# Optimization experiments

Measured on AMD Instinct MI355X. Metric: run time of the kernel, lower is better.

Reference implementation:

```python
import jax, jax.numpy as jnp
import numpy as np

N = 50000      # nodes
E = 800000     # edges (avg degree 16)
D_IN, D_H, D_OUT = 128, 256, 128


def setup_inputs() -> dict:
    key = jax.random.key(0)
    ks = jax.random.split(key, 8)
    x = jax.random.normal(ks[0], (N, D_IN), dtype=jnp.float32)
    edge_index = jax.random.randint(ks[1], (2, E), 0, N, dtype=jnp.int64)
    s1 = 1.0 / np.sqrt(D_IN).astype(np.float32)
    s2 = 1.0 / np.sqrt(D_H).astype(np.float32)
    return {
        "x": x,
        "edge_index": edge_index,
        "W1l": jax.random.normal(ks[2], (D_H, D_IN), jnp.float32) * s1,
        "b1l": jnp.zeros((D_H,), jnp.float32),
        "W1r": jax.random.normal(ks[3], (D_H, D_IN), jnp.float32) * s1,
        "W2l": jax.random.normal(ks[4], (D_OUT, D_H), jnp.float32) * s2,
        "b2l": jnp.zeros((D_OUT,), jnp.float32),
        "W2r": jax.random.normal(ks[5], (D_OUT, D_H), jnp.float32) * s2,
    }


def sage_conv(x, src, dst, Wl, bl, Wr):
    # mean-aggregate source features into destination nodes
    agg = jax.ops.segment_sum(x[src], dst, num_segments=N)           # [N, d_in]
    deg = jax.ops.segment_sum(jnp.ones((src.shape[0],), x.dtype), dst, num_segments=N)
    mean = agg / jnp.maximum(deg, 1.0)[:, None]
    # lin_l(mean_agg) + lin_r(x_root); lin_r has no bias (PyG SAGEConv default)
    return mean @ Wl.T + bl + x @ Wr.T


def reference(x, edge_index, W1l, b1l, W1r, W2l, b2l, W2r):
    src, dst = edge_index[0], edge_index[1]
    h = sage_conv(x, src, dst, W1l, b1l, W1r)
    h = jax.nn.relu(h)  # dropout inactive in eval mode
    return sage_conv(h, src, dst, W2l, b2l, W2r)
```

## Files before the change

### kernel.cpp

```cpp
#include <hip/hip_runtime.h>


typedef __attribute__((ext_vector_type(8))) short bf16x8;
typedef __attribute__((ext_vector_type(4))) float floatx4;

__device__ inline unsigned short f2b(float f) {
  unsigned int x = __float_as_uint(f);
  unsigned int r = (x + 0x7fffu + ((x >> 16) & 1u)) >> 16;
  return (unsigned short)r;
}
__device__ inline float blo(unsigned int u) { return __uint_as_float(u << 16); }
__device__ inline float bhi(unsigned int u) { return __uint_as_float(u & 0xffff0000u); }

__global__ void prep_kernel(const float* __restrict__ x,
                            const float* __restrict__ W1l, const float* __restrict__ W1r,
                            const float* __restrict__ W2l, const float* __restrict__ W2r,
                            unsigned short* __restrict__ Wc1, unsigned short* __restrict__ Wc2,
                            unsigned short* __restrict__ A1,
                            int* __restrict__ cnt, int* __restrict__ off, int N, int E) {
  int i = blockIdx.x * blockDim.x + threadIdx.x;
  if (i < 65536) {
    int j = i >> 8, k = i & 255;
    float v1 = (k < 128) ? W1l[j * 128 + k] : W1r[j * 128 + (k - 128)];
    Wc1[i] = f2b(v1);
    float v2 = (j < 128) ? W2l[j * 256 + k] : W2r[(j - 128) * 256 + k];
    Wc2[i] = f2b(v2);
  }
  if (i < N) cnt[i] = 0;
  if (i == 0) off[N] = E;
  if (i < N * 32) {
    int n = i >> 5, c = (i & 31) * 4;
    float4 v = *(const float4*)(x + (size_t)n * 128 + c);
    uint2 p;
    p.x = (unsigned int)f2b(v.x) | ((unsigned int)f2b(v.y) << 16);
    p.y = (unsigned int)f2b(v.z) | ((unsigned int)f2b(v.w) << 16);
    *(uint2*)(A1 + (size_t)n * 256 + 128 + c) = p;
  }
}

__global__ void hist_kernel(const int* __restrict__ dst, int* __restrict__ cnt,
                            int* __restrict__ rank, int E) {
  int i = blockIdx.x * blockDim.x + threadIdx.x;
  int e = i * 4;
  if (e + 3 < E) {
    int4 d = *(const int4*)(dst + e);
    int4 r;
    r.x = atomicAdd(&cnt[d.x], 1);
    r.y = atomicAdd(&cnt[d.y], 1);
    r.z = atomicAdd(&cnt[d.z], 1);
    r.w = atomicAdd(&cnt[d.w], 1);
    *(int4*)(rank + e) = r;
  } else {
    for (; e < E; e++) rank[e] = atomicAdd(&cnt[dst[e]], 1);
  }
}

__global__ __launch_bounds__(1024) void scan_blocks_kernel(const int* __restrict__ cnt,
                                                           int* __restrict__ off,
                                                           int* __restrict__ bsum, int N) {
  __shared__ int wsum[16];
  __shared__ int wincl[16];
  const int tid = threadIdx.x;
  const int lane = tid & 63;
  const int wv = tid >> 6;
  const int i = blockIdx.x * 1024 + tid;
  const int v = (i < N) ? cnt[i] : 0;
  int s = v;
#pragma unroll
  for (int o = 1; o < 64; o <<= 1) {
    int t = __shfl_up(s, o, 64);
    if (lane >= o) s += t;
  }
  if (lane == 63) wsum[wv] = s;
  __syncthreads();
  if (tid < 16) {
    int ws = wsum[tid];
#pragma unroll
    for (int o = 1; o < 16; o <<= 1) {
      int t = __shfl_up(ws, o, 16);
      if ((tid & 15) >= o) ws += t;
    }
    wincl[tid] = ws;
  }
  __syncthreads();
  const int wo = wv ? wincl[wv - 1] : 0;
  if (i < N) off[i] = wo + s - v;
  if (tid == 1023) bsum[blockIdx.x] = wo + s;
}

__global__ __launch_bounds__(1024) void scan_add_kernel(int* __restrict__ off,
                                                        const int* __restrict__ bsum, int N, int SB) {
  __shared__ int bofs[64];
  const int tid = threadIdx.x;
  if (tid < 64) {
    int v = (tid < SB) ? bsum[tid] : 0;
    int s = v;
#pragma unroll
    for (int o = 1; o < 64; o <<= 1) {
      int t = __shfl_up(s, o, 64);
      if (tid >= o) s += t;
    }
    bofs[tid] = s - v;
  }
  __syncthreads();
  int i = blockIdx.x * 1024 + tid;
  if (i < N) off[i] = off[i] + bofs[blockIdx.x];
}

__global__ void fill_kernel(const int* __restrict__ src, const int* __restrict__ dst,
                            const int* __restrict__ rank, const int* __restrict__ off,
                            int* __restrict__ csr, int E) {
  int i = blockIdx.x * blockDim.x + threadIdx.x;
  int e = i * 4;
  if (e + 3 < E) {
    int4 d = *(const int4*)(dst + e);
    int4 r = *(const int4*)(rank + e);
    int4 s = *(const int4*)(src + e);
    csr[off[d.x] + r.x] = s.x;
    csr[off[d.y] + r.y] = s.y;
    csr[off[d.z] + r.z] = s.z;
    csr[off[d.w] + r.w] = s.w;
  } else {
    for (; e < E; e++) csr[off[dst[e]] + rank[e]] = src[e];
  }
}

__global__ void gather1_kernel(const unsigned short* __restrict__ feat,
                               const int* __restrict__ csr, const int* __restrict__ off,
                               unsigned short* __restrict__ ob, int N) {
  int wid = (blockIdx.x * blockDim.x + threadIdx.x) >> 6;
  if (wid >= N) return;
  const int lane = threadIdx.x & 63;
  const int s0 = off[wid], s1 = off[wid + 1];
  float a0 = 0.f, a1 = 0.f;
  for (int base = s0; base < s1; base += 64) {
    const int cnt = min(64, s1 - base);
    int my = (lane < cnt) ? csr[base + lane] : 0;
    int k = 0;
    for (; k + 8 <= cnt; k += 8) {
      int i0 = __shfl(my, k);
      int i1 = __shfl(my, k + 1);
      int i2 = __shfl(my, k + 2);
      int i3 = __shfl(my, k + 3);
      int i4 = __shfl(my, k + 4);
      int i5 = __shfl(my, k + 5);
      int i6 = __shfl(my, k + 6);
      int i7 = __shfl(my, k + 7);
      unsigned u0 = ((const unsigned*)(feat + (size_t)i0 * 256))[lane];
      unsigned u1 = ((const unsigned*)(feat + (size_t)i1 * 256))[lane];
      unsigned u2 = ((const unsigned*)(feat + (size_t)i2 * 256))[lane];
      unsigned u3 = ((const unsigned*)(feat + (size_t)i3 * 256))[lane];
      unsigned u4 = ((const unsigned*)(feat + (size_t)i4 * 256))[lane];
      unsigned u5 = ((const unsigned*)(feat + (size_t)i5 * 256))[lane];
      unsigned u6 = ((const unsigned*)(feat + (size_t)i6 * 256))[lane];
      unsigned u7 = ((const unsigned*)(feat + (size_t)i7 * 256))[lane];
      a0 += blo(u0); a1 += bhi(u0);
      a0 += blo(u1); a1 += bhi(u1);
      a0 += blo(u2); a1 += bhi(u2);
      a0 += blo(u3); a1 += bhi(u3);
      a0 += blo(u4); a1 += bhi(u4);
      a0 += blo(u5); a1 += bhi(u5);
      a0 += blo(u6); a1 += bhi(u6);
      a0 += blo(u7); a1 += bhi(u7);
    }
    for (; k + 2 <= cnt; k += 2) {
      int i0 = __shfl(my, k);
      int i1 = __shfl(my, k + 1);
      unsigned u0 = ((const unsigned*)(feat + (size_t)i0 * 256))[lane];
      unsigned u1 = ((const unsigned*)(feat + (size_t)i1 * 256))[lane];
      a0 += blo(u0); a1 += bhi(u0);
      a0 += blo(u1); a1 += bhi(u1);
    }
    if (k < cnt) {
      int i0 = __shfl(my, k);
      unsigned u0 = ((const unsigned*)(feat + (size_t)i0 * 256))[lane];
      a0 += blo(u0); a1 += bhi(u0);
    }
  }
  const float inv = 1.0f / fmaxf((float)(s1 - s0), 1.0f);
  unsigned p = (unsigned)f2b(a0 * inv) | ((unsigned)f2b(a1 * inv) << 16);
  ((unsigned*)(ob + (size_t)wid * 256))[lane] = p;
}

__global__ void gather2_kernel(const unsigned short* __restrict__ t,
                               const int* __restrict__ csr, const int* __restrict__ off,
                               float* __restrict__ out, int N) {
  int wid = (blockIdx.x * blockDim.x + threadIdx.x) >> 6;
  if (wid >= N) return;
  const int lane = threadIdx.x & 63;
  const int s0 = off[wid], s1 = off[wid + 1];
  float2* op = (float2*)(out + (size_t)wid * 128) + lane;
  float2 r = *op;
  float a0 = 0.f, a1 = 0.f;
  for (int base = s0; base < s1; base += 64) {
    const int cnt = min(64, s1 - base);
    int my = (lane < cnt) ? csr[base + lane] : 0;
    int k = 0;
    for (; k + 8 <= cnt; k += 8) {
      int i0 = __shfl(my, k);
      int i1 = __shfl(my, k + 1);
      int i2 = __shfl(my, k + 2);
      int i3 = __shfl(my, k + 3);
      int i4 = __shfl(my, k + 4);
      int i5 = __shfl(my, k + 5);
      int i6 = __shfl(my, k + 6);
      int i7 = __shfl(my, k + 7);
      unsigned u0 = ((const unsigned*)(t + (size_t)i0 * 128))[lane];
      unsigned u1 = ((const unsigned*)(t + (size_t)i1 * 128))[lane];
      unsigned u2 = ((const unsigned*)(t + (size_t)i2 * 128))[lane];
      unsigned u3 = ((const unsigned*)(t + (size_t)i3 * 128))[lane];
      unsigned u4 = ((const unsigned*)(t + (size_t)i4 * 128))[lane];
      unsigned u5 = ((const unsigned*)(t + (size_t)i5 * 128))[lane];
      unsigned u6 = ((const unsigned*)(t + (size_t)i6 * 128))[lane];
      unsigned u7 = ((const unsigned*)(t + (size_t)i7 * 128))[lane];
      a0 += blo(u0); a1 += bhi(u0);
      a0 += blo(u1); a1 += bhi(u1);
      a0 += blo(u2); a1 += bhi(u2);
      a0 += blo(u3); a1 += bhi(u3);
      a0 += blo(u4); a1 += bhi(u4);
      a0 += blo(u5); a1 += bhi(u5);
      a0 += blo(u6); a1 += bhi(u6);
      a0 += blo(u7); a1 += bhi(u7);
    }
    for (; k + 2 <= cnt; k += 2) {
      int i0 = __shfl(my, k);
      int i1 = __shfl(my, k + 1);
      unsigned u0 = ((const unsigned*)(t + (size_t)i0 * 128))[lane];
      unsigned u1 = ((const unsigned*)(t + (size_t)i1 * 128))[lane];
      a0 += blo(u0); a1 += bhi(u0);
      a0 += blo(u1); a1 += bhi(u1);
    }
    if (k < cnt) {
      int i0 = __shfl(my, k);
      unsigned u0 = ((const unsigned*)(t + (size_t)i0 * 128))[lane];
      a0 += blo(u0); a1 += bhi(u0);
    }
  }
  const float inv = 1.0f / fmaxf((float)(s1 - s0), 1.0f);
  r.x += a0 * inv;
  r.y += a1 * inv;
  *op = r;
}

__global__ __launch_bounds__(512, 4)
void gemm_fused(const unsigned short* __restrict__ A, const unsigned short* __restrict__ Wc1,
                const unsigned short* __restrict__ Wc2,
                const float* __restrict__ b1, const float* __restrict__ b2,
                unsigned short* __restrict__ tb, float* __restrict__ out, int M) {
  constexpr int LDA = 264;
  __shared__ __align__(16) unsigned short As[64 * LDA];
  __shared__ __align__(16) unsigned short Hs[64 * LDA];
  const int t = threadIdx.x;
  const int lane = t & 63;
  const int wave = t >> 6;
  const int wn = wave * 32;
  const int l15 = lane & 15;
  const int quad = lane >> 4;
  const int m_blk = blockIdx.x * 64;

  bf16x8 wr[2][8];
#pragma unroll
  for (int nt = 0; nt < 2; nt++) {
    const unsigned short* wp = Wc1 + (size_t)(wn + nt * 16 + l15) * 256 + quad * 8;
#pragma unroll
    for (int c = 0; c < 8; c++) wr[nt][c] = *(const bf16x8*)(wp + c * 32);
  }
  const float bv0 = b1[wn + l15];
  const float bv1 = b1[wn + 16 + l15];

#pragma unroll
  for (int i = 0; i < 4; i++) {
    int idx = t + 512 * i;
    int row = idx >> 5, cc = (idx & 31) * 8;
    int ar = m_blk + row;
    if (ar >= M) ar = M - 1;
    *(uint4*)(As + row * LDA + cc) = *(const uint4*)(A + (size_t)ar * 256 + cc);
  }
  __syncthreads();

  floatx4 acc[4][2] = {};
#pragma unroll
  for (int c = 0; c < 8; c++) {
    bf16x8 af[4];
#pragma unroll
    for (int mt = 0; mt < 4; mt++)
      af[mt] = *(const bf16x8*)(As + (mt * 16 + l15) * LDA + c * 32 + quad * 8);
#pragma unroll
    for (int mt = 0; mt < 4; mt++) {
      acc[mt][0] = __builtin_amdgcn_mfma_f32_16x16x32_bf16(af[mt], wr[0][c], acc[mt][0], 0, 0, 0);
      acc[mt][1] = __builtin_amdgcn_mfma_f32_16x16x32_bf16(af[mt], wr[1][c], acc[mt][1], 0, 0, 0);
    }
  }

#pragma unroll
  for (int mt = 0; mt < 4; mt++) {
#pragma unroll
    for (int nt = 0; nt < 2; nt++) {
      const int jl = wn + nt * 16 + l15;
      const float bv = nt ? bv1 : bv0;
#pragma unroll
      for (int r = 0; r < 4; r++) {
        const int row = mt * 16 + quad * 4 + r;
        Hs[row * LDA + jl] = f2b(fmaxf(acc[mt][nt][r] + bv, 0.f));
      }
    }
  }

#pragma unroll
  for (int nt = 0; nt < 2; nt++) {
    const unsigned short* wp = Wc2 + (size_t)(wn + nt * 16 + l15) * 256 + quad * 8;
#pragma unroll
    for (int c = 0; c < 8; c++) wr[nt][c] = *(const bf16x8*)(wp + c * 32);
  }
  const float cv0 = (wn >= 128) ? b2[wn - 128 + l15] : 0.f;
  const float cv1 = (wn >= 128) ? b2[wn - 112 + l15] : 0.f;
  __syncthreads();

#pragma unroll
  for (int mt = 0; mt < 4; mt++) {
    acc[mt][0] = (floatx4){0.f, 0.f, 0.f, 0.f};
    acc[mt][1] = (floatx4){0.f, 0.f, 0.f, 0.f};
  }
#pragma unroll
  for (int c = 0; c < 8; c++) {
    bf16x8 af[4];
#pragma unroll
    for (int mt = 0; mt < 4; mt++)
      af[mt] = *(const bf16x8*)(Hs + (mt * 16 + l15) * LDA + c * 32 + quad * 8);
#pragma unroll
    for (int mt = 0; mt < 4; mt++) {
      acc[mt][0] = __builtin_amdgcn_mfma_f32_16x16x32_bf16(af[mt], wr[0][c], acc[mt][0], 0, 0, 0);
      acc[mt][1] = __builtin_amdgcn_mfma_f32_16x16x32_bf16(af[mt], wr[1][c], acc[mt][1], 0, 0, 0);
    }
  }

#pragma unroll
  for (int mt = 0; mt < 4; mt++) {
#pragma unroll
    for (int nt = 0; nt < 2; nt++) {
      const int j = wn + nt * 16 + l15;
      const float bv = nt ? cv1 : cv0;
#pragma unroll
      for (int r = 0; r < 4; r++) {
        const int node = m_blk + mt * 16 + quad * 4 + r;
        if (node >= M) continue;
        const float v = acc[mt][nt][r];
        if (j < 128) {
          tb[(size_t)node * 128 + j] = f2b(v);
        } else {
          out[(size_t)node * 128 + (j - 128)] = v + bv;
        }
      }
    }
  }
}

extern "C" void kernel_launch(void* const* d_in, const int* in_sizes, int n_in,
                              void* d_out, int out_size, void* d_ws, size_t ws_size,
                              hipStream_t stream) {
  const float* x   = (const float*)d_in[0];
  const int*  eidx = (const int*)d_in[1];
  const float* W1l = (const float*)d_in[2];
  const float* b1l = (const float*)d_in[3];
  const float* W1r = (const float*)d_in[4];
  const float* W2l = (const float*)d_in[5];
  const float* b2l = (const float*)d_in[6];
  const float* W2r = (const float*)d_in[7];
  float* out = (float*)d_out;

  const int N = in_sizes[0] / 128;
  const int E = in_sizes[1] / 2;
  const int* src = eidx;
  const int* dst = eidx + E;

  int* cnt  = (int*)d_ws;
  int* off  = cnt + N;
  int* bsum = off + N + 1;
  int* rank = bsum + 64;
  int* csr  = rank + E;
  size_t ioff = ((size_t)(N + N + 1 + 64 + 2 * E) * 4 + 15) & ~(size_t)15;
  unsigned short* A1  = (unsigned short*)((char*)d_ws + ioff);
  unsigned short* tb  = A1 + (size_t)N * 256;
  unsigned short* Wc1 = tb + (size_t)N * 128;
  unsigned short* Wc2 = Wc1 + 65536;

  const int SB = (N + 1023) / 1024;

  prep_kernel<<<(N * 32 + 255) / 256, 256, 0, stream>>>(x, W1l, W1r, W2l, W2r,
                                                        Wc1, Wc2, A1, cnt, off, N, E);
  hist_kernel<<<(E / 4 + 255) / 256, 256, 0, stream>>>(dst, cnt, rank, E);
  scan_blocks_kernel<<<SB, 1024, 0, stream>>>(cnt, off, bsum, N);
  scan_add_kernel<<<SB, 1024, 0, stream>>>(off, bsum, N, SB);
  fill_kernel<<<(E / 4 + 255) / 256, 256, 0, stream>>>(src, dst, rank, off, csr, E);

  const int gblocks = (N + 3) / 4;
  gather1_kernel<<<gblocks, 256, 0, stream>>>(A1 + 128, csr, off, A1, N);

  gemm_fused<<<(N + 63) / 64, 512, 0, stream>>>(A1, Wc1, Wc2, b1l, b2l, tb, out, N);

  gather2_kernel<<<gblocks, 256, 0, stream>>>(tb, csr, off, out, N);
}
```

Measured before the change: 265.8 us.

## Merge LDS tiles, swap MFMA operands for vector stores, halve weight registers

The fused two-layer GEMM kernel now uses one shared LDS buffer for the input tile and the hidden tile instead of two, halving LDS per block. Weight fragments are loaded in two K-halves of four chunks each, halving the weight registers held per thread. MFMA operands are swapped so each lane holds four consecutive output columns, which allows packed uint2 bf16 stores and float4 fp32 stores in place of scalar ones. The global loads of A are issued before the weight loads to overlap latency, and sched_barriers are added, at the cost of an extra barrier and a reload of weights in mid-loop.

```diff
diff --git a/kernel.cpp b/kernel.cpp
--- a/kernel.cpp
+++ b/kernel.cpp
@@ -248,8 +248,7 @@
                 const float* __restrict__ b1, const float* __restrict__ b2,
                 unsigned short* __restrict__ tb, float* __restrict__ out, int M) {
   constexpr int LDA = 264;
-  __shared__ __align__(16) unsigned short As[64 * LDA];
-  __shared__ __align__(16) unsigned short Hs[64 * LDA];
+  __shared__ __align__(16) unsigned short AH[64 * LDA];
   const int t = threadIdx.x;
   const int lane = t & 63;
   const int wave = t >> 6;
@@ -258,62 +257,96 @@
   const int quad = lane >> 4;
   const int m_blk = blockIdx.x * 64;
 
-  bf16x8 wr[2][8];
+  uint4 sv[4];
+  int srow[4], scol[4];
+#pragma unroll
+  for (int i = 0; i < 4; i++) {
+    int idx = t + 512 * i;
+    srow[i] = idx >> 5;
+    scol[i] = (idx & 31) * 8;
+    int ar = m_blk + srow[i];
+    if (ar >= M) ar = M - 1;
+    sv[i] = *(const uint4*)(A + (size_t)ar * 256 + scol[i]);
+  }
+
+  bf16x8 wr[2][4];
 #pragma unroll
   for (int nt = 0; nt < 2; nt++) {
     const unsigned short* wp = Wc1 + (size_t)(wn + nt * 16 + l15) * 256 + quad * 8;
 #pragma unroll
-    for (int c = 0; c < 8; c++) wr[nt][c] = *(const bf16x8*)(wp + c * 32);
-  }
-  const float bv0 = b1[wn + l15];
-  const float bv1 = b1[wn + 16 + l15];
-
-#pragma unroll
-  for (int i = 0; i < 4; i++) {
-    int idx = t + 512 * i;
-    int row = idx >> 5, cc = (idx & 31) * 8;
-    int ar = m_blk + row;
-    if (ar >= M) ar = M - 1;
-    *(uint4*)(As + row * LDA + cc) = *(const uint4*)(A + (size_t)ar * 256 + cc);
-  }
+    for (int c = 0; c < 4; c++) wr[nt][c] = *(const bf16x8*)(wp + c * 32);
+  }
+  float4 bq[2];
+#pragma unroll
+  for (int nt = 0; nt < 2; nt++)
+    bq[nt] = *(const float4*)(b1 + wn + nt * 16 + quad * 4);
+
+#pragma unroll
+  for (int i = 0; i < 4; i++)
+    *(uint4*)(AH + srow[i] * LDA + scol[i]) = sv[i];
   __syncthreads();
 
   floatx4 acc[4][2] = {};
-#pragma unroll
-  for (int c = 0; c < 8; c++) {
+
+#pragma unroll
+  for (int c = 0; c < 4; c++) {
     bf16x8 af[4];
 #pragma unroll
     for (int mt = 0; mt < 4; mt++)
-      af[mt] = *(const bf16x8*)(As + (mt * 16 + l15) * LDA + c * 32 + quad * 8);
+      af[mt] = *(const bf16x8*)(AH + (mt * 16 + l15) * LDA + c * 32 + quad * 8);
 #pragma unroll
     for (int mt = 0; mt < 4; mt++) {
-      acc[mt][0] = __builtin_amdgcn_mfma_f32_16x16x32_bf16(af[mt], wr[0][c], acc[mt][0], 0, 0, 0);
-      acc[mt][1] = __builtin_amdgcn_mfma_f32_16x16x32_bf16(af[mt], wr[1][c], acc[mt][1], 0, 0, 0);
-    }
-  }
-
-#pragma unroll
-  for (int mt = 0; mt < 4; mt++) {
-#pragma unroll
-    for (int nt = 0; nt < 2; nt++) {
-      const int jl = wn + nt * 16 + l15;
-      const float bv = nt ? bv1 : bv0;
-#pragma unroll
-      for (int r = 0; r < 4; r++) {
-        const int row = mt * 16 + quad * 4 + r;
-        Hs[row * LDA + jl] = f2b(fmaxf(acc[mt][nt][r] + bv, 0.f));
-      }
-    }
-  }
-
+      acc[mt][0] = __builtin_amdgcn_mfma_f32_16x16x32_bf16(wr[0][c], af[mt], acc[mt][0], 0, 0, 0);
+      acc[mt][1] = __builtin_amdgcn_mfma_f32_16x16x32_bf16(wr[1][c], af[mt], acc[mt][1], 0, 0, 0);
+    }
+  }
+  __builtin_amdgcn_sched_barrier(0);
+#pragma unroll
+  for (int nt = 0; nt < 2; nt++) {
+    const unsigned short* wp = Wc1 + (size_t)(wn + nt * 16 + l15) * 256 + 128 + quad * 8;
+#pragma unroll
+    for (int c = 0; c < 4; c++) wr[nt][c] = *(const bf16x8*)(wp + c * 32);
+  }
+#pragma unroll
+  for (int c = 0; c < 4; c++) {
+    bf16x8 af[4];
+#pragma unroll
+    for (int mt = 0; mt < 4; mt++)
+      af[mt] = *(const bf16x8*)(AH + (mt * 16 + l15) * LDA + 128 + c * 32 + quad * 8);
+#pragma unroll
+    for (int mt = 0; mt < 4; mt++) {
+      acc[mt][0] = __builtin_amdgcn_mfma_f32_16x16x32_bf16(wr[0][c], af[mt], acc[mt][0], 0, 0, 0);
+      acc[mt][1] = __builtin_amdgcn_mfma_f32_16x16x32_bf16(wr[1][c], af[mt], acc[mt][1], 0, 0, 0);
+    }
+  }
+  __builtin_amdgcn_sched_barrier(0);
 #pragma unroll
   for (int nt = 0; nt < 2; nt++) {
     const unsigned short* wp = Wc2 + (size_t)(wn + nt * 16 + l15) * 256 + quad * 8;
 #pragma unroll
-    for (int c = 0; c < 8; c++) wr[nt][c] = *(const bf16x8*)(wp + c * 32);
-  }
-  const float cv0 = (wn >= 128) ? b2[wn - 128 + l15] : 0.f;
-  const float cv1 = (wn >= 128) ? b2[wn - 112 + l15] : 0.f;
+    for (int c = 0; c < 4; c++) wr[nt][c] = *(const bf16x8*)(wp + c * 32);
+  }
+  __syncthreads();
+
+#pragma unroll
+  for (int mt = 0; mt < 4; mt++) {
+#pragma unroll
+    for (int nt = 0; nt < 2; nt++) {
+      const int node = mt * 16 + l15;
+      const int j0 = wn + nt * 16 + quad * 4;
+      uint2 p;
+      p.x = (unsigned)f2b(fmaxf(acc[mt][nt][0] + bq[nt].x, 0.f)) |
+            ((unsigned)f2b(fmaxf(acc[mt][nt][1] + bq[nt].y, 0.f)) << 16);
+      p.y = (unsigned)f2b(fmaxf(acc[mt][nt][2] + bq[nt].z, 0.f)) |
+            ((unsigned)f2b(fmaxf(acc[mt][nt][3] + bq[nt].w, 0.f)) << 16);
+      *(uint2*)(AH + node * LDA + j0) = p;
+    }
+  }
+  if (wn >= 128) {
+#pragma unroll
+    for (int nt = 0; nt < 2; nt++)
+      bq[nt] = *(const float4*)(b2 + wn - 128 + nt * 16 + quad * 4);
+  }
   __syncthreads();
 
 #pragma unroll
@@ -322,34 +355,56 @@
     acc[mt][1] = (floatx4){0.f, 0.f, 0.f, 0.f};
   }
 #pragma unroll
-  for (int c = 0; c < 8; c++) {
-    bf16x8 af[4];
+  for (int c = 0; c < 4; c++) {
+    bf16x8 hf[4];
 #pragma unroll
     for (int mt = 0; mt < 4; mt++)
-      af[mt] = *(const bf16x8*)(Hs + (mt * 16 + l15) * LDA + c * 32 + quad * 8);
+      hf[mt] = *(const bf16x8*)(AH + (mt * 16 + l15) * LDA + c * 32 + quad * 8);
 #pragma unroll
     for (int mt = 0; mt < 4; mt++) {
-      acc[mt][0] = __builtin_amdgcn_mfma_f32_16x16x32_bf16(af[mt], wr[0][c], acc[mt][0], 0, 0, 0);
-      acc[mt][1] = __builtin_amdgcn_mfma_f32_16x16x32_bf16(af[mt], wr[1][c], acc[mt][1], 0, 0, 0);
+      acc[mt][0] = __builtin_amdgcn_mfma_f32_16x16x32_bf16(wr[0][c], hf[mt], acc[mt][0], 0, 0, 0);
+      acc[mt][1] = __builtin_amdgcn_mfma_f32_16x16x32_bf16(wr[1][c], hf[mt], acc[mt][1], 0, 0, 0);
+    }
+  }
+  __builtin_amdgcn_sched_barrier(0);
+#pragma unroll
+  for (int nt = 0; nt < 2; nt++) {
+    const unsigned short* wp = Wc2 + (size_t)(wn + nt * 16 + l15) * 256 + 128 + quad * 8;
+#pragma unroll
+    for (int c = 0; c < 4; c++) wr[nt][c] = *(const bf16x8*)(wp + c * 32);
+  }
+#pragma unroll
+  for (int c = 0; c < 4; c++) {
+    bf16x8 hf[4];
+#pragma unroll
+    for (int mt = 0; mt < 4; mt++)
+      hf[mt] = *(const bf16x8*)(AH + (mt * 16 + l15) * LDA + 128 + c * 32 + quad * 8);
+#pragma unroll
+    for (int mt = 0; mt < 4; mt++) {
+      acc[mt][0] = __builtin_amdgcn_mfma_f32_16x16x32_bf16(wr[0][c], hf[mt], acc[mt][0], 0, 0, 0);
+      acc[mt][1] = __builtin_amdgcn_mfma_f32_16x16x32_bf16(wr[1][c], hf[mt], acc[mt][1], 0, 0, 0);
     }
   }
 
 #pragma unroll
   for (int mt = 0; mt < 4; mt++) {
+    const int node = m_blk + mt * 16 + l15;
+    if (node >= M) continue;
 #pragma unroll
     for (int nt = 0; nt < 2; nt++) {
-      const int j = wn + nt * 16 + l15;
-      const float bv = nt ? cv1 : cv0;
-#pragma unroll
-      for (int r = 0; r < 4; r++) {
-        const int node = m_blk + mt * 16 + quad * 4 + r;
-        if (node >= M) continue;
-        const float v = acc[mt][nt][r];
-        if (j < 128) {
-          tb[(size_t)node * 128 + j] = f2b(v);
-        } else {
-          out[(size_t)node * 128 + (j - 128)] = v + bv;
-        }
+      const int j0 = wn + nt * 16 + quad * 4;
+      if (wn < 128) {
+        uint2 p;
+        p.x = (unsigned)f2b(acc[mt][nt][0]) | ((unsigned)f2b(acc[mt][nt][1]) << 16);
+        p.y = (unsigned)f2b(acc[mt][nt][2]) | ((unsigned)f2b(acc[mt][nt][3]) << 16);
+        *(uint2*)(tb + (size_t)node * 128 + j0) = p;
+      } else {
+        float4 o;
+        o.x = acc[mt][nt][0] + bq[nt].x;
+        o.y = acc[mt][nt][1] + bq[nt].y;
+        o.z = acc[mt][nt][2] + bq[nt].z;
+        o.w = acc[mt][nt][3] + bq[nt].w;
+        *(float4*)(out + (size_t)node * 128 + (j0 - 128)) = o;
       }
     }
   }
```

Measured after the change: 267.0 us. Within noise of the previous version (+0.5%).
